# Kernel tuning notes

Hardware: AMD Instinct MI355X
Metric: run time of the kernel (lower is better)

Reference implementation:

```python
import jax, jax.numpy as jnp
import numpy as np

EMBED = 1024
HIDDEN = 4 * EMBED
EPS = 1e-5

def _layer_norm(x, g, b):
    mu = jnp.mean(x, axis=-1, keepdims=True)
    var = jnp.mean((x - mu) ** 2, axis=-1, keepdims=True)
    return (x - mu) * jax.lax.rsqrt(var + EPS) * g + b

def setup_inputs() -> dict:
    key = jax.random.key(0)
    ks = jax.random.split(key, 8)
    s = 1.0 / np.sqrt(EMBED)
    inp = {
        "x": jax.random.normal(ks[0], (4, 2048, EMBED), dtype=jnp.float32),
        "Wq": jax.random.normal(ks[1], (EMBED, EMBED), dtype=jnp.float32) * s,
        "bq": jnp.zeros((EMBED,), jnp.float32),
        "Wk": jax.random.normal(ks[2], (EMBED, EMBED), dtype=jnp.float32) * s,
        "bk": jnp.zeros((EMBED,), jnp.float32),
        "Wv": jax.random.normal(ks[3], (EMBED, EMBED), dtype=jnp.float32) * s,
        "bv": jnp.zeros((EMBED,), jnp.float32),
        "W1": jax.random.normal(ks[4], (EMBED, HIDDEN), dtype=jnp.float32) * s,
        "b1": jnp.zeros((HIDDEN,), jnp.float32),
        "W2": jax.random.normal(ks[5], (HIDDEN, EMBED), dtype=jnp.float32) * (1.0 / np.sqrt(HIDDEN)),
        "b2": jnp.zeros((EMBED,), jnp.float32),
        "g1": jnp.ones((EMBED,), jnp.float32),
        "be1": jnp.zeros((EMBED,), jnp.float32),
        "g2": jnp.ones((EMBED,), jnp.float32),
        "be2": jnp.zeros((EMBED,), jnp.float32),
    }
    return inp

def reference(x, Wq, bq, Wk, bk, Wv, bv, W1, b1, W2, b2, g1, be1, g2, be2):
    # pre-norm attention
    h = _layer_norm(x, g1, be1)
    Q = h @ Wq + bq  # [B,S,D]
    K = h @ Wk + bk
    V = h @ Wv + bv
    scale = 1.0 / jnp.sqrt(jnp.asarray(EMBED, x.dtype))
    scores = jnp.einsum('bqd,bkd->bqk', Q, K) * scale  # [B,S,S]
    weights = jax.nn.softmax(scores, axis=-1)
    attn = jnp.einsum('bqk,bkd->bqd', weights, V)
    x = x + attn
    # pre-norm MLP
    h2 = _layer_norm(x, g2, be2)
    ff = jax.nn.relu(h2 @ W1 + b1) @ W2 + b2
    return x + ff
```

## Files before the change

kernel.cpp:

```cpp
#include <hip/hip_runtime.h>

#define EMBED 1024
#define HID   4096
#define NB    4
#define SEQ   2048

typedef __attribute__((ext_vector_type(8))) __bf16 bf16x8;
typedef __attribute__((ext_vector_type(4))) float  f32x4;
typedef __attribute__((ext_vector_type(4))) int    i32x4;
typedef unsigned short u16;

__device__ __forceinline__ u16 f2bf(float f) {
  unsigned u = __float_as_uint(f);
  u += 0x7FFFu + ((u >> 16) & 1u);
  return (u16)(u >> 16);
}

typedef const __attribute__((address_space(1))) unsigned int* gas_t;
typedef __attribute__((address_space(3))) unsigned int* las_t;
__device__ __forceinline__ void gld16(const void* g, void* l) {
  __builtin_amdgcn_global_load_lds((gas_t)g, (las_t)l, 16, 0, 0);
}

#define RD16(p)       __builtin_bit_cast(bf16x8, *(const i32x4*)(p))
#define MFMA16(a,b,c) __builtin_amdgcn_mfma_f32_16x16x32_bf16(a, b, c, 0, 0, 0)

template<int EPI>
__global__ __launch_bounds__(512, 2) void gemm8p(
    const u16* __restrict__ A, int lda, long long astr,
    const u16* __restrict__ B, int ldb, long long bstr,
    void* __restrict__ C, int ldc, long long cstr,
    const float* __restrict__ bias,
    const float* __restrict__ add,
    float scale, int Kdim)
{
  __shared__ i32x4 lds4[9216];
  const int SLOT = 49152;

  const int tid  = threadIdx.x;
  const int lane = tid & 63;
  const int w    = tid >> 6;
  const int wr   = w >> 1, wc = w & 1;
  const int l15  = lane & 15, l4 = lane >> 4;

  const int gx   = gridDim.x;
  const int nwg  = gx * gridDim.y;
  const int orig = blockIdx.y * gx + blockIdx.x;
  const int t    = ((nwg & 7) == 0) ? ((orig & 7) * (nwg >> 3) + (orig >> 3)) : orig;
  const int bx   = t % gx, by = t / gx;

  const u16* Ab = A + (size_t)blockIdx.z * astr + (size_t)by * 256 * lda;
  const u16* Bb = B + (size_t)blockIdx.z * bstr + (size_t)bx * 128 * ldb;

  size_t gaoff[4], gboff[2];
  #pragma unroll
  for (int i = 0; i < 4; ++i) {
    const int idx = i * 512 + tid, row = idx >> 3, gc = (idx & 7) ^ (row & 7);
    gaoff[i] = (size_t)row * lda + gc * 8;
  }
  #pragma unroll
  for (int j = 0; j < 2; ++j) {
    const int idx = j * 512 + tid, row = idx >> 3, gc = (idx & 7) ^ (row & 7);
    gboff[j] = (size_t)row * ldb + gc * 8;
  }

  int aoff[4], boff[4], cp16[2];
  #pragma unroll
  for (int m = 0; m < 4; ++m) aoff[m] = (wr * 64 + m * 16 + l15) * 128;
  #pragma unroll
  for (int n = 0; n < 4; ++n) boff[n] = 32768 + (wc * 64 + n * 16 + l15) * 128;
  cp16[0] = ((0 + l4) ^ (l15 & 7)) * 16;
  cp16[1] = ((4 + l4) ^ (l15 & 7)) * 16;

  f32x4 acc[4][4] = {};
  const int NT = Kdim >> 6;
  char* lbase = (char*)lds4;

  {
    char* s0 = lbase;
    char* s1 = lbase + SLOT;
    #pragma unroll
    for (int i = 0; i < 4; ++i) gld16(Ab + gaoff[i],      s0 + (i * 512 + w * 64) * 16);
    #pragma unroll
    for (int j = 0; j < 2; ++j) gld16(Bb + gboff[j],      s0 + 32768 + (j * 512 + w * 64) * 16);
    #pragma unroll
    for (int i = 0; i < 4; ++i) gld16(Ab + gaoff[i] + 64, s1 + (i * 512 + w * 64) * 16);
    #pragma unroll
    for (int j = 0; j < 2; ++j) gld16(Bb + gboff[j] + 64, s1 + 32768 + (j * 512 + w * 64) * 16);
  }

  int s = 0;
  for (int T = 0; T < NT; ++T) {
    const bool st  = (T + 2 < NT);
    const size_t kk = (size_t)(T + 2) * 64;
    const char* rA = lbase + s * SLOT;
    char* wS = lbase + ((s + 2 >= 3) ? (s - 1) : (s + 2)) * SLOT;

    if (T == NT - 1) asm volatile("s_waitcnt vmcnt(0)" ::: "memory");
    else             asm volatile("s_waitcnt vmcnt(6)" ::: "memory");
    __builtin_amdgcn_s_barrier();
    __builtin_amdgcn_sched_barrier(0);

    bf16x8 b0, b1, b2, b3, a0, a1;

    b0 = RD16(rA + boff[0] + cp16[0]);
    b1 = RD16(rA + boff[1] + cp16[0]);
    b2 = RD16(rA + boff[2] + cp16[0]);
    b3 = RD16(rA + boff[3] + cp16[0]);
    a0 = RD16(rA + aoff[0] + cp16[0]);
    a1 = RD16(rA + aoff[1] + cp16[0]);
    if (st) {
      gld16(Ab + gaoff[0] + kk, wS + (0 * 512 + w * 64) * 16);
      gld16(Ab + gaoff[1] + kk, wS + (1 * 512 + w * 64) * 16);
    }
    __builtin_amdgcn_s_barrier();
    asm volatile("s_waitcnt lgkmcnt(0)" ::: "memory");
    __builtin_amdgcn_sched_barrier(0);
    __builtin_amdgcn_s_setprio(1);
    acc[0][0] = MFMA16(a0, b0, acc[0][0]);
    acc[0][1] = MFMA16(a0, b1, acc[0][1]);
    acc[0][2] = MFMA16(a0, b2, acc[0][2]);
    acc[0][3] = MFMA16(a0, b3, acc[0][3]);
    acc[1][0] = MFMA16(a1, b0, acc[1][0]);
    acc[1][1] = MFMA16(a1, b1, acc[1][1]);
    acc[1][2] = MFMA16(a1, b2, acc[1][2]);
    acc[1][3] = MFMA16(a1, b3, acc[1][3]);
    __builtin_amdgcn_s_setprio(0);

    a0 = RD16(rA + aoff[2] + cp16[0]);
    a1 = RD16(rA + aoff[3] + cp16[0]);
    if (st) {
      gld16(Ab + gaoff[2] + kk, wS + (2 * 512 + w * 64) * 16);
      gld16(Ab + gaoff[3] + kk, wS + (3 * 512 + w * 64) * 16);
    }
    __builtin_amdgcn_s_barrier();
    asm volatile("s_waitcnt lgkmcnt(0)" ::: "memory");
    __builtin_amdgcn_sched_barrier(0);
    __builtin_amdgcn_s_setprio(1);
    acc[2][0] = MFMA16(a0, b0, acc[2][0]);
    acc[2][1] = MFMA16(a0, b1, acc[2][1]);
    acc[2][2] = MFMA16(a0, b2, acc[2][2]);
    acc[2][3] = MFMA16(a0, b3, acc[2][3]);
    acc[3][0] = MFMA16(a1, b0, acc[3][0]);
    acc[3][1] = MFMA16(a1, b1, acc[3][1]);
    acc[3][2] = MFMA16(a1, b2, acc[3][2]);
    acc[3][3] = MFMA16(a1, b3, acc[3][3]);
    __builtin_amdgcn_s_setprio(0);

    b0 = RD16(rA + boff[0] + cp16[1]);
    b1 = RD16(rA + boff[1] + cp16[1]);
    b2 = RD16(rA + boff[2] + cp16[1]);
    b3 = RD16(rA + boff[3] + cp16[1]);
    a0 = RD16(rA + aoff[0] + cp16[1]);
    a1 = RD16(rA + aoff[1] + cp16[1]);
    if (st) {
      gld16(Bb + gboff[0] + kk, wS + 32768 + (0 * 512 + w * 64) * 16);
    }
    __builtin_amdgcn_s_barrier();
    asm volatile("s_waitcnt lgkmcnt(0)" ::: "memory");
    __builtin_amdgcn_sched_barrier(0);
    __builtin_amdgcn_s_setprio(1);
    acc[0][0] = MFMA16(a0, b0, acc[0][0]);
    acc[0][1] = MFMA16(a0, b1, acc[0][1]);
    acc[0][2] = MFMA16(a0, b2, acc[0][2]);
    acc[0][3] = MFMA16(a0, b3, acc[0][3]);
    acc[1][0] = MFMA16(a1, b0, acc[1][0]);
    acc[1][1] = MFMA16(a1, b1, acc[1][1]);
    acc[1][2] = MFMA16(a1, b2, acc[1][2]);
    acc[1][3] = MFMA16(a1, b3, acc[1][3]);
    __builtin_amdgcn_s_setprio(0);

    a0 = RD16(rA + aoff[2] + cp16[1]);
    a1 = RD16(rA + aoff[3] + cp16[1]);
    if (st) {
      gld16(Bb + gboff[1] + kk, wS + 32768 + (1 * 512 + w * 64) * 16);
    }
    __builtin_amdgcn_s_barrier();
    asm volatile("s_waitcnt lgkmcnt(0)" ::: "memory");
    __builtin_amdgcn_sched_barrier(0);
    __builtin_amdgcn_s_setprio(1);
    acc[2][0] = MFMA16(a0, b0, acc[2][0]);
    acc[2][1] = MFMA16(a0, b1, acc[2][1]);
    acc[2][2] = MFMA16(a0, b2, acc[2][2]);
    acc[2][3] = MFMA16(a0, b3, acc[2][3]);
    acc[3][0] = MFMA16(a1, b0, acc[3][0]);
    acc[3][1] = MFMA16(a1, b1, acc[3][1]);
    acc[3][2] = MFMA16(a1, b2, acc[3][2]);
    acc[3][3] = MFMA16(a1, b3, acc[3][3]);
    __builtin_amdgcn_s_setprio(0);

    s = (s + 1 == 3) ? 0 : s + 1;
  }

  const int bm0 = by * 256 + wr * 64;
  const int bn0 = bx * 128 + wc * 64;
  float* Cf = (float*)C;
  u16*   Ch = (u16*)C;
  #pragma unroll
  for (int mi = 0; mi < 4; ++mi) {
    #pragma unroll
    for (int ni = 0; ni < 4; ++ni) {
      const int col = bn0 + ni * 16 + l15;
      const int r0  = bm0 + mi * 16 + l4 * 4;
      float bv = 0.f;
      if (EPI == 0 || EPI == 3 || EPI == 4) bv = bias[col];
      #pragma unroll
      for (int r = 0; r < 4; ++r) {
        const size_t idx = (size_t)blockIdx.z * cstr + (size_t)(r0 + r) * ldc + col;
        const float v = acc[mi][ni][r];
        if      (EPI == 0) Ch[idx] = f2bf(v + bv);
        else if (EPI == 1) Cf[idx] = v * scale;
        else if (EPI == 2) Cf[idx] = v + add[idx];
        else if (EPI == 3) Ch[idx] = f2bf(fmaxf(v + bv, 0.f));
        else               Cf[idx] = v + bv + add[idx];
      }
    }
  }
}

__global__ __launch_bounds__(256) void ln_kernel(
    const float* __restrict__ x, const float* __restrict__ g,
    const float* __restrict__ be, u16* __restrict__ out)
{
  const int row = blockIdx.x;
  const int tid = threadIdx.x;
  const float4 v = ((const float4*)(x + (size_t)row * EMBED))[tid];
  float s  = v.x + v.y + v.z + v.w;
  float s2 = v.x * v.x + v.y * v.y + v.z * v.z + v.w * v.w;
  #pragma unroll
  for (int m = 1; m < 64; m <<= 1) { s += __shfl_xor(s, m); s2 += __shfl_xor(s2, m); }
  __shared__ float ls[4], ls2[4];
  const int w = tid >> 6;
  if ((tid & 63) == 0) { ls[w] = s; ls2[w] = s2; }
  __syncthreads();
  s  = ls[0] + ls[1] + ls[2] + ls[3];
  s2 = ls2[0] + ls2[1] + ls2[2] + ls2[3];
  const float mu   = s * (1.f / EMBED);
  const float var  = s2 * (1.f / EMBED) - mu * mu;
  const float rstd = rsqrtf(var + 1e-5f);
  const float4 gv = ((const float4*)g)[tid];
  const float4 bv = ((const float4*)be)[tid];
  ushort4 o;
  o.x = f2bf((v.x - mu) * rstd * gv.x + bv.x);
  o.y = f2bf((v.y - mu) * rstd * gv.y + bv.y);
  o.z = f2bf((v.z - mu) * rstd * gv.z + bv.z);
  o.w = f2bf((v.w - mu) * rstd * gv.w + bv.w);
  ((ushort4*)(out + (size_t)row * EMBED))[tid] = o;
}

__global__ __launch_bounds__(256) void softmax_kernel(
    const float* __restrict__ S, u16* __restrict__ P)
{
  const int tid = threadIdx.x;
  const size_t base = ((size_t)blockIdx.y * SEQ + blockIdx.x) * SEQ;
  const float4* src = (const float4*)(S + base);
  float4 a = src[tid];
  float4 b = src[tid + 256];
  float m = fmaxf(fmaxf(fmaxf(a.x, a.y), fmaxf(a.z, a.w)),
                  fmaxf(fmaxf(b.x, b.y), fmaxf(b.z, b.w)));
  #pragma unroll
  for (int msk = 1; msk < 64; msk <<= 1) m = fmaxf(m, __shfl_xor(m, msk));
  __shared__ float red[8];
  const int w = tid >> 6;
  if ((tid & 63) == 0) red[w] = m;
  __syncthreads();
  m = fmaxf(fmaxf(red[0], red[1]), fmaxf(red[2], red[3]));
  a.x = __expf(a.x - m); a.y = __expf(a.y - m); a.z = __expf(a.z - m); a.w = __expf(a.w - m);
  b.x = __expf(b.x - m); b.y = __expf(b.y - m); b.z = __expf(b.z - m); b.w = __expf(b.w - m);
  float s = a.x + a.y + a.z + a.w + b.x + b.y + b.z + b.w;
  #pragma unroll
  for (int msk = 1; msk < 64; msk <<= 1) s += __shfl_xor(s, msk);
  if ((tid & 63) == 0) red[4 + w] = s;
  __syncthreads();
  s = red[4] + red[5] + red[6] + red[7];
  const float inv = 1.0f / s;
  ushort4 oa, ob;
  oa.x = f2bf(a.x * inv); oa.y = f2bf(a.y * inv); oa.z = f2bf(a.z * inv); oa.w = f2bf(a.w * inv);
  ob.x = f2bf(b.x * inv); ob.y = f2bf(b.y * inv); ob.z = f2bf(b.z * inv); ob.w = f2bf(b.w * inv);
  ushort4* dst = (ushort4*)(P + base);
  dst[tid]       = oa;
  dst[tid + 256] = ob;
}

__global__ void transpose_cast_f32(const float* __restrict__ W, u16* __restrict__ Wt,
                                   int K, int N)
{
  __shared__ float t[32][33];
  const int tx = threadIdx.x, ty = threadIdx.y;
  const int n0 = blockIdx.x * 32, k0 = blockIdx.y * 32;
  #pragma unroll
  for (int i = 0; i < 4; ++i)
    t[ty + i * 8][tx] = W[(size_t)(k0 + ty + i * 8) * N + n0 + tx];
  __syncthreads();
  #pragma unroll
  for (int i = 0; i < 4; ++i)
    Wt[(size_t)(n0 + ty + i * 8) * K + k0 + tx] = f2bf(t[tx][ty + i * 8]);
}

__global__ void transpose_bf16(const u16* __restrict__ V, u16* __restrict__ Vt,
                               int sld, long long sstr, long long dstr)
{
  __shared__ u16 t[32][33];
  const int tx = threadIdx.x, ty = threadIdx.y;
  const int d0 = blockIdx.x * 32, s0 = blockIdx.y * 32;
  const size_t so = (size_t)blockIdx.z * sstr;
  const size_t do_ = (size_t)blockIdx.z * dstr;
  #pragma unroll
  for (int i = 0; i < 4; ++i)
    t[ty + i * 8][tx] = V[so + (size_t)(s0 + ty + i * 8) * sld + d0 + tx];
  __syncthreads();
  #pragma unroll
  for (int i = 0; i < 4; ++i)
    Vt[do_ + (size_t)(d0 + ty + i * 8) * SEQ + s0 + tx] = t[tx][ty + i * 8];
}

__global__ void concat_bias(const float* __restrict__ a, const float* __restrict__ b,
                            const float* __restrict__ c, float* __restrict__ o)
{
  const int i = blockIdx.x * 1024 + threadIdx.x;
  o[i] = (i < 1024) ? a[i] : (i < 2048) ? b[i - 1024] : c[i - 2048];
}

extern "C" void kernel_launch(void* const* d_in, const int* in_sizes, int n_in,
                              void* d_out, int out_size, void* d_ws, size_t ws_size,
                              hipStream_t stream)
{
  const float* x   = (const float*)d_in[0];
  const float* Wq  = (const float*)d_in[1];
  const float* bq  = (const float*)d_in[2];
  const float* Wk  = (const float*)d_in[3];
  const float* bk  = (const float*)d_in[4];
  const float* Wv  = (const float*)d_in[5];
  const float* bv  = (const float*)d_in[6];
  const float* W1  = (const float*)d_in[7];
  const float* b1  = (const float*)d_in[8];
  const float* W2  = (const float*)d_in[9];
  const float* b2  = (const float*)d_in[10];
  const float* g1  = (const float*)d_in[11];
  const float* be1 = (const float*)d_in[12];
  const float* g2  = (const float*)d_in[13];
  const float* be2 = (const float*)d_in[14];
  float* out = (float*)d_out;

  const size_t RD = (size_t)NB * SEQ * EMBED;

  char* base = (char*)d_ws;
  size_t o = 0;
  auto alloc = [&](size_t bytes) -> void* {
    o = (o + 255) & ~(size_t)255;
    void* p = base + o;
    o += bytes;
    return p;
  };

  u16*   wqkvT = (u16*)alloc((size_t)3 * EMBED * EMBED * 2);
  u16*   w1T   = (u16*)alloc((size_t)HID * EMBED * 2);
  u16*   w2T   = (u16*)alloc((size_t)EMBED * HID * 2);
  float* bqkv  = (float*)alloc(3072 * 4);
  u16*   h     = (u16*)alloc(RD * 2);
  u16*   QKV   = (u16*)alloc(RD * 3 * 2);
  u16*   Vt    = (u16*)alloc(RD * 2);
  float* x2    = (float*)alloc(RD * 4);

  const size_t need_batched = o + (size_t)NB * SEQ * SEQ * 6 + 1024;
  const int NZ = (ws_size >= need_batched) ? NB : 1;
  float* Sbuf = (float*)alloc((size_t)NZ * SEQ * SEQ * 4);
  u16*   Pb   = (u16*)alloc((size_t)NZ * SEQ * SEQ * 2);
  u16*   ff   = (NZ == NB) ? (u16*)Sbuf
                           : (u16*)alloc((size_t)NB * SEQ * HID * 2);

  const dim3 blk(512);
  const dim3 tblk(32, 8);

  transpose_cast_f32<<<dim3(32, 32), tblk, 0, stream>>>(Wq, wqkvT, EMBED, EMBED);
  transpose_cast_f32<<<dim3(32, 32), tblk, 0, stream>>>(Wk, wqkvT + (size_t)EMBED * EMBED, EMBED, EMBED);
  transpose_cast_f32<<<dim3(32, 32), tblk, 0, stream>>>(Wv, wqkvT + (size_t)2 * EMBED * EMBED, EMBED, EMBED);
  transpose_cast_f32<<<dim3(HID / 32, EMBED / 32), tblk, 0, stream>>>(W1, w1T, EMBED, HID);
  transpose_cast_f32<<<dim3(EMBED / 32, HID / 32), tblk, 0, stream>>>(W2, w2T, HID, EMBED);
  concat_bias<<<dim3(3), dim3(1024), 0, stream>>>(bq, bk, bv, bqkv);

  ln_kernel<<<dim3(NB * SEQ), dim3(256), 0, stream>>>(x, g1, be1, h);

  gemm8p<0><<<dim3(3072 / 128, NB * SEQ / 256, 1), blk, 0, stream>>>(
      h, EMBED, 0LL, wqkvT, EMBED, 0LL, QKV, 3072, 0LL, bqkv, nullptr, 1.f, EMBED);

  transpose_bf16<<<dim3(EMBED / 32, SEQ / 32, NB), tblk, 0, stream>>>(
      QKV + 2048, Vt, 3072, (long long)SEQ * 3072, (long long)EMBED * SEQ);

  for (int b = 0; b < NB; b += NZ) {
    const u16* Qp  = QKV + (size_t)b * SEQ * 3072;
    const u16* Kp  = Qp + 1024;
    const u16* Vtp = Vt + (size_t)b * EMBED * SEQ;
    float* x2p     = x2 + (size_t)b * SEQ * EMBED;
    const float* xp = x + (size_t)b * SEQ * EMBED;
    gemm8p<1><<<dim3(SEQ / 128, SEQ / 256, NZ), blk, 0, stream>>>(
        Qp, 3072, (long long)SEQ * 3072, Kp, 3072, (long long)SEQ * 3072,
        Sbuf, SEQ, (long long)SEQ * SEQ, nullptr, nullptr, 0.03125f, EMBED);
    softmax_kernel<<<dim3(SEQ, NZ), dim3(256), 0, stream>>>(Sbuf, Pb);
    gemm8p<2><<<dim3(EMBED / 128, SEQ / 256, NZ), blk, 0, stream>>>(
        Pb, SEQ, (long long)SEQ * SEQ, Vtp, SEQ, (long long)EMBED * SEQ,
        x2p, EMBED, (long long)SEQ * EMBED, nullptr, xp, 1.f, SEQ);
  }

  ln_kernel<<<dim3(NB * SEQ), dim3(256), 0, stream>>>(x2, g2, be2, h);

  gemm8p<3><<<dim3(HID / 128, NB * SEQ / 256, 1), blk, 0, stream>>>(
      h, EMBED, 0LL, w1T, EMBED, 0LL, ff, HID, 0LL, b1, nullptr, 1.f, EMBED);
  gemm8p<4><<<dim3(EMBED / 128, NB * SEQ / 256, 1), blk, 0, stream>>>(
      ff, HID, 0LL, w2T, HID, 0LL, out, EMBED, 0LL, b2, x2, 1.f, HID);
}
```

Baseline: 363.9 us.

## Add 256x256-tile double-buffered GEMM kernel for QKV, scores and FFN1

Introduces a new gemm256 kernel with 256x256 output tiles, 8 waves arranged 2x4, an XOR-swizzled LDS layout, a two-buffer 128KB LDS pipeline with phased global-to-LDS loads, and an XCD-aware block remap. It replaces the 256x128 gemm8p for the QKV projection, the attention score GEMM and the first MLP GEMM, aiming to raise arithmetic intensity and cut LDS/global traffic per FLOP. The larger tile halves the grid size and 128KB LDS limits occupancy to one block per CU, which can hurt latency hiding and tail utilisation. Barrier macros are also introduced in the old kernel without behaviour change.

```diff
diff --git a/kernel.cpp b/kernel.cpp
--- a/kernel.cpp
+++ b/kernel.cpp
@@ -24,6 +24,152 @@
 
 #define RD16(p)       __builtin_bit_cast(bf16x8, *(const i32x4*)(p))
 #define MFMA16(a,b,c) __builtin_amdgcn_mfma_f32_16x16x32_bf16(a, b, c, 0, 0, 0)
+#define SCHED0()      __builtin_amdgcn_sched_barrier(0)
+#define BARR()        __builtin_amdgcn_s_barrier()
+#define LGKM0()       asm volatile("s_waitcnt lgkmcnt(0)" ::: "memory")
+#define VMW(n)        asm volatile("s_waitcnt vmcnt(" #n ")" ::: "memory")
+
+template<int EPI>
+__global__ __launch_bounds__(512, 2) void gemm256(
+    const u16* __restrict__ A, int lda, long long astr,
+    const u16* __restrict__ B, int ldb, long long bstr,
+    void* __restrict__ C, int ldc, long long cstr,
+    const float* __restrict__ bias,
+    const float* __restrict__ add,
+    float scale, int Kdim)
+{
+  __shared__ char lds[131072];
+
+  const int tid  = threadIdx.x;
+  const int lane = tid & 63;
+  const int w    = tid >> 6;
+  const int wr   = w >> 2, wc = w & 3;
+  const int l15  = lane & 15, l4 = lane >> 4;
+
+  const int gx   = gridDim.x;
+  const int nwg  = gx * gridDim.y;
+  const int orig = blockIdx.y * gx + blockIdx.x;
+  const int t    = ((nwg & 7) == 0) ? ((orig & 7) * (nwg >> 3) + (orig >> 3)) : orig;
+  const int bx   = t % gx, by = t / gx;
+
+  const u16* Ab = A + (size_t)blockIdx.z * astr + (size_t)by * 256 * lda;
+  const u16* Bb = B + (size_t)blockIdx.z * bstr + (size_t)bx * 256 * ldb;
+
+  const int    srow = tid >> 3;
+  const size_t sa   = (size_t)srow * lda + (size_t)(((tid & 7) ^ (srow & 7)) * 8);
+  const size_t sb   = (size_t)srow * ldb + (size_t)(((tid & 7) ^ (srow & 7)) * 8);
+  const int    ldst = tid * 16;
+
+  auto stA = [&](int buf, int q, int kk) {
+    gld16(Ab + (size_t)(q * 64) * lda + kk + sa, lds + buf * 65536 + q * 8192 + ldst);
+  };
+  auto stB = [&](int buf, int i, int kk) {
+    gld16(Bb + (size_t)(i * 64) * ldb + kk + sb, lds + buf * 65536 + 32768 + i * 8192 + ldst);
+  };
+
+  const int arow = (wr * 128 + l15) * 128;
+  const int brow = 32768 + (wc * 64 + l15) * 128;
+  const int cp0  = ((0 + l4) ^ (l15 & 7)) * 16;
+  const int cp1  = ((4 + l4) ^ (l15 & 7)) * 16;
+
+  f32x4 acc[8][4] = {};
+  bf16x8 a0, a1, a2, a3, b0, b1, b2, b3, b4, b5, b6, b7;
+
+  const int NT = Kdim >> 6;
+  const int NI = NT >> 1;
+
+#define BLOADS(LB) \
+    b0 = RD16((LB) + brow + 0 * 2048 + cp0); \
+    b1 = RD16((LB) + brow + 1 * 2048 + cp0); \
+    b2 = RD16((LB) + brow + 2 * 2048 + cp0); \
+    b3 = RD16((LB) + brow + 3 * 2048 + cp0); \
+    b4 = RD16((LB) + brow + 0 * 2048 + cp1); \
+    b5 = RD16((LB) + brow + 1 * 2048 + cp1); \
+    b6 = RD16((LB) + brow + 2 * 2048 + cp1); \
+    b7 = RD16((LB) + brow + 3 * 2048 + cp1);
+
+#define PHASE(LB, MP, PRE, STG, VMST) do { \
+    a0 = RD16((LB) + arow + (MP) * 4096 + cp0); \
+    a1 = RD16((LB) + arow + (MP) * 4096 + cp1); \
+    a2 = RD16((LB) + arow + (MP) * 4096 + 2048 + cp0); \
+    a3 = RD16((LB) + arow + (MP) * 4096 + 2048 + cp1); \
+    PRE STG VMST \
+    SCHED0(); BARR(); LGKM0(); SCHED0(); \
+    __builtin_amdgcn_s_setprio(1); \
+    acc[2*(MP)  ][0] = MFMA16(a0, b0, acc[2*(MP)  ][0]); \
+    acc[2*(MP)  ][1] = MFMA16(a0, b1, acc[2*(MP)  ][1]); \
+    acc[2*(MP)  ][2] = MFMA16(a0, b2, acc[2*(MP)  ][2]); \
+    acc[2*(MP)  ][3] = MFMA16(a0, b3, acc[2*(MP)  ][3]); \
+    acc[2*(MP)+1][0] = MFMA16(a2, b0, acc[2*(MP)+1][0]); \
+    acc[2*(MP)+1][1] = MFMA16(a2, b1, acc[2*(MP)+1][1]); \
+    acc[2*(MP)+1][2] = MFMA16(a2, b2, acc[2*(MP)+1][2]); \
+    acc[2*(MP)+1][3] = MFMA16(a2, b3, acc[2*(MP)+1][3]); \
+    acc[2*(MP)  ][0] = MFMA16(a1, b4, acc[2*(MP)  ][0]); \
+    acc[2*(MP)  ][1] = MFMA16(a1, b5, acc[2*(MP)  ][1]); \
+    acc[2*(MP)  ][2] = MFMA16(a1, b6, acc[2*(MP)  ][2]); \
+    acc[2*(MP)  ][3] = MFMA16(a1, b7, acc[2*(MP)  ][3]); \
+    acc[2*(MP)+1][0] = MFMA16(a3, b4, acc[2*(MP)+1][0]); \
+    acc[2*(MP)+1][1] = MFMA16(a3, b5, acc[2*(MP)+1][1]); \
+    acc[2*(MP)+1][2] = MFMA16(a3, b6, acc[2*(MP)+1][2]); \
+    acc[2*(MP)+1][3] = MFMA16(a3, b7, acc[2*(MP)+1][3]); \
+    __builtin_amdgcn_s_setprio(0); \
+    SCHED0(); BARR(); SCHED0(); \
+  } while (0)
+
+  stB(0, 0, 0); stB(0, 1, 0); stB(0, 2, 0); stB(0, 3, 0);
+  stA(0, 0, 0); stA(0, 1, 0); stA(0, 2, 0); stA(0, 3, 0);
+  stB(1, 0, 64); stB(1, 1, 64); stB(1, 2, 64); stB(1, 3, 64);
+  stA(1, 0, 64); stA(1, 2, 64);
+  VMW(6);
+  BARR(); SCHED0();
+
+  const char* L0 = lds;
+  const char* L1 = lds + 65536;
+
+  for (int I = 0; I < NI; ++I) {
+    const bool st = (I + 1 < NI);
+    const int k1 = (2 * I + 1) * 64;
+    const int k2 = (2 * I + 2) * 64;
+    const int k3 = (2 * I + 3) * 64;
+
+    PHASE(L0, 0, BLOADS(L0), { stA(1, 1, k1); stA(1, 3, k1); }, ;);
+    PHASE(L0, 1, ;, if (st) { stB(0, 0, k2); stB(0, 1, k2); }, ;);
+    PHASE(L0, 2, ;, if (st) { stB(0, 2, k2); stB(0, 3, k2); }, ;);
+    if (st) { PHASE(L0, 3, ;, { stA(0, 0, k2); stA(0, 2, k2); }, VMW(6);); }
+    else    { PHASE(L0, 3, ;, ;, VMW(0);); }
+    PHASE(L1, 0, BLOADS(L1), if (st) { stA(0, 1, k2); stA(0, 3, k2); }, ;);
+    PHASE(L1, 1, ;, if (st) { stB(1, 0, k3); stB(1, 1, k3); }, ;);
+    PHASE(L1, 2, ;, if (st) { stB(1, 2, k3); stB(1, 3, k3); }, ;);
+    if (st) { PHASE(L1, 3, ;, { stA(1, 0, k3); stA(1, 2, k3); }, VMW(6);); }
+    else    { PHASE(L1, 3, ;, ;, ;); }
+  }
+#undef PHASE
+#undef BLOADS
+
+  const int bm0 = by * 256 + wr * 128;
+  const int bn0 = bx * 256 + wc * 64;
+  float* Cf = (float*)C;
+  u16*   Ch = (u16*)C;
+  #pragma unroll
+  for (int mi = 0; mi < 8; ++mi) {
+    #pragma unroll
+    for (int ni = 0; ni < 4; ++ni) {
+      const int col = bn0 + ni * 16 + l15;
+      const int r0  = bm0 + mi * 16 + l4 * 4;
+      float bv = 0.f;
+      if (EPI == 0 || EPI == 3 || EPI == 4) bv = bias[col];
+      #pragma unroll
+      for (int r = 0; r < 4; ++r) {
+        const size_t idx = (size_t)blockIdx.z * cstr + (size_t)(r0 + r) * ldc + col;
+        const float v = acc[mi][ni][r];
+        if      (EPI == 0) Ch[idx] = f2bf(v + bv);
+        else if (EPI == 1) Cf[idx] = v * scale;
+        else if (EPI == 3) Ch[idx] = f2bf(fmaxf(v + bv, 0.f));
+        else if (EPI == 4) Cf[idx] = v + bv + add[idx];
+      }
+    }
+  }
+}
 
 template<int EPI>
 __global__ __launch_bounds__(512, 2) void gemm8p(
@@ -98,8 +244,8 @@
 
     if (T == NT - 1) asm volatile("s_waitcnt vmcnt(0)" ::: "memory");
     else             asm volatile("s_waitcnt vmcnt(6)" ::: "memory");
-    __builtin_amdgcn_s_barrier();
-    __builtin_amdgcn_sched_barrier(0);
+    BARR();
+    SCHED0();
 
     bf16x8 b0, b1, b2, b3, a0, a1;
 
@@ -113,9 +259,9 @@
       gld16(Ab + gaoff[0] + kk, wS + (0 * 512 + w * 64) * 16);
       gld16(Ab + gaoff[1] + kk, wS + (1 * 512 + w * 64) * 16);
     }
-    __builtin_amdgcn_s_barrier();
-    asm volatile("s_waitcnt lgkmcnt(0)" ::: "memory");
-    __builtin_amdgcn_sched_barrier(0);
+    BARR();
+    LGKM0();
+    SCHED0();
     __builtin_amdgcn_s_setprio(1);
     acc[0][0] = MFMA16(a0, b0, acc[0][0]);
     acc[0][1] = MFMA16(a0, b1, acc[0][1]);
@@ -133,9 +279,9 @@
       gld16(Ab + gaoff[2] + kk, wS + (2 * 512 + w * 64) * 16);
       gld16(Ab + gaoff[3] + kk, wS + (3 * 512 + w * 64) * 16);
     }
-    __builtin_amdgcn_s_barrier();
-    asm volatile("s_waitcnt lgkmcnt(0)" ::: "memory");
-    __builtin_amdgcn_sched_barrier(0);
+    BARR();
+    LGKM0();
+    SCHED0();
     __builtin_amdgcn_s_setprio(1);
     acc[2][0] = MFMA16(a0, b0, acc[2][0]);
     acc[2][1] = MFMA16(a0, b1, acc[2][1]);
@@ -156,9 +302,9 @@
     if (st) {
       gld16(Bb + gboff[0] + kk, wS + 32768 + (0 * 512 + w * 64) * 16);
     }
-    __builtin_amdgcn_s_barrier();
-    asm volatile("s_waitcnt lgkmcnt(0)" ::: "memory");
-    __builtin_amdgcn_sched_barrier(0);
+    BARR();
+    LGKM0();
+    SCHED0();
     __builtin_amdgcn_s_setprio(1);
     acc[0][0] = MFMA16(a0, b0, acc[0][0]);
     acc[0][1] = MFMA16(a0, b1, acc[0][1]);
@@ -175,9 +321,9 @@
     if (st) {
       gld16(Bb + gboff[1] + kk, wS + 32768 + (1 * 512 + w * 64) * 16);
     }
-    __builtin_amdgcn_s_barrier();
-    asm volatile("s_waitcnt lgkmcnt(0)" ::: "memory");
-    __builtin_amdgcn_sched_barrier(0);
+    BARR();
+    LGKM0();
+    SCHED0();
     __builtin_amdgcn_s_setprio(1);
     acc[2][0] = MFMA16(a0, b0, acc[2][0]);
     acc[2][1] = MFMA16(a0, b1, acc[2][1]);
@@ -381,7 +527,7 @@
 
   ln_kernel<<<dim3(NB * SEQ), dim3(256), 0, stream>>>(x, g1, be1, h);
 
-  gemm8p<0><<<dim3(3072 / 128, NB * SEQ / 256, 1), blk, 0, stream>>>(
+  gemm256<0><<<dim3(3072 / 256, NB * SEQ / 256, 1), blk, 0, stream>>>(
       h, EMBED, 0LL, wqkvT, EMBED, 0LL, QKV, 3072, 0LL, bqkv, nullptr, 1.f, EMBED);
 
   transpose_bf16<<<dim3(EMBED / 32, SEQ / 32, NB), tblk, 0, stream>>>(
@@ -393,7 +539,7 @@
     const u16* Vtp = Vt + (size_t)b * EMBED * SEQ;
     float* x2p     = x2 + (size_t)b * SEQ * EMBED;
     const float* xp = x + (size_t)b * SEQ * EMBED;
-    gemm8p<1><<<dim3(SEQ / 128, SEQ / 256, NZ), blk, 0, stream>>>(
+    gemm256<1><<<dim3(SEQ / 256, SEQ / 256, NZ), blk, 0, stream>>>(
         Qp, 3072, (long long)SEQ * 3072, Kp, 3072, (long long)SEQ * 3072,
         Sbuf, SEQ, (long long)SEQ * SEQ, nullptr, nullptr, 0.03125f, EMBED);
     softmax_kernel<<<dim3(SEQ, NZ), dim3(256), 0, stream>>>(Sbuf, Pb);
@@ -404,7 +550,7 @@
 
   ln_kernel<<<dim3(NB * SEQ), dim3(256), 0, stream>>>(x2, g2, be2, h);
 
-  gemm8p<3><<<dim3(HID / 128, NB * SEQ / 256, 1), blk, 0, stream>>>(
+  gemm256<3><<<dim3(HID / 256, NB * SEQ / 256, 1), blk, 0, stream>>>(
       h, EMBED, 0LL, w1T, EMBED, 0LL, ff, HID, 0LL, b1, nullptr, 1.f, EMBED);
   gemm8p<4><<<dim3(EMBED / 128, NB * SEQ / 256, 1), blk, 0, stream>>>(
       ff, HID, 0LL, w2T, HID, 0LL, out, EMBED, 0LL, b2, x2, 1.f, HID);
```

Result: no change. 364.9 us (+0.3%).
